# Performance work log

Hardware: AMD Instinct MI355X
Metric: run time of the kernel (lower is better)

Reference implementation:

```python
import jax, jax.numpy as jnp
import numpy as np

N = 4096        # num_node == num_hyperedge
IN_FT = 512
OUT_FT = 512
COS_THR = 0.5
COS_K = 10
SCALER = 1.0
EPS = 1e-12  # torch F.normalize eps


def _kaiming_uniform(key, shape, fan_in, a=2.0):
    # kaiming_uniform_ with a=sqrt(4)=2: gain = sqrt(2/(1+a^2)), bound = gain*sqrt(3/fan_in)
    gain = np.sqrt(2.0 / (1.0 + a * a))
    bound = gain * np.sqrt(3.0 / fan_in)
    return jax.random.uniform(key, shape, jnp.float32, -bound, bound)


def setup_inputs() -> dict:
    key = jax.random.key(0)
    k_x, k_w1, k_w2, k_pw, k_pb = jax.random.split(key, 5)
    x = jax.random.normal(k_x, (N, IN_FT), jnp.float32)
    H = jnp.ones((N, N), jnp.float32)  # initial full incidence, sparsified in forward
    weight1 = jnp.abs(_kaiming_uniform(k_w1, (N, N), fan_in=N))
    weight2 = jnp.abs(_kaiming_uniform(k_w2, (N, N), fan_in=N))
    proj_w = _kaiming_uniform(k_pw, (OUT_FT, IN_FT), fan_in=IN_FT)
    b = 1.0 / np.sqrt(IN_FT)
    proj_b = jax.random.uniform(k_pb, (OUT_FT,), jnp.float32, -b, b)
    return {"x": x, "H": H, "proj_w": proj_w, "proj_b": proj_b,
            "weight1": weight1, "weight2": weight2}


def reference(x, H, proj_w, proj_b, weight1, weight2):
    # --- dynamic hypergraph construction: cosine similarity + threshold/top-k mask ---
    xn = x / jnp.maximum(jnp.linalg.norm(x, axis=1, keepdims=True), 1e-12)
    cos = xn @ xn.T                                  # [N, N]
    mask = cos > COS_THR
    _, idx = jax.lax.top_k(cos, COS_K)               # [N, K] top-k per row
    rows = jnp.arange(N)[:, None]
    mask = mask.at[rows, idx].set(True)
    Hm = H * mask.astype(H.dtype)                    # sparsified incidence

    # --- projection ---
    h = x @ proj_w.T + proj_b                        # [N, out_ft]

    # --- node -> hyperedge aggregation ---
    nw = (weight1 * Hm).T                            # [E, N]
    nw = nw / jnp.maximum(jnp.sum(jnp.abs(nw), axis=1, keepdims=True), EPS) * SCALER
    h = nw @ h                                       # [E, out_ft]

    # --- hyperedge -> node aggregation ---
    hw = weight2 * Hm                                # [N, E]
    hw = hw / jnp.maximum(jnp.sum(jnp.abs(hw), axis=1, keepdims=True), EPS) * SCALER
    return hw @ h                                    # [N, out_ft]
```

## Files before the change

### kernel.cpp

```cpp
#include <hip/hip_runtime.h>
#include <hip/hip_bf16.h>
#include <math.h>

#define N 4096
#define IN_FT 512
#define OUT_FT 512
#define COS_THR 0.5f
#define COS_K 10
#define EPSN 1e-12f
#define CAP 256
#define NW (N / 32)
#define CAP_C 128
#define GAPWIN 1e-2f
#define CNB 32
#define T0 0.08f
#define SLOTS 24
#define NSLOT (32 * SLOTS)

typedef short s16x8 __attribute__((ext_vector_type(8)));
typedef float f32x4 __attribute__((ext_vector_type(4)));

__device__ __forceinline__ unsigned short f2bf(float f) {
    unsigned u = __float_as_uint(f);
    u += 0x7fff + ((u >> 16) & 1);
    return (unsigned short)(u >> 16);
}
__device__ __forceinline__ float bf2f(unsigned short h) {
    return __uint_as_float(((unsigned)h) << 16);
}
__device__ __forceinline__ void gload_lds16(const void* g, void* l) {
    __builtin_amdgcn_global_load_lds(
        (const __attribute__((address_space(1))) void*)g,
        (__attribute__((address_space(3))) void*)l, 16, 0, 0);
}

__global__ __launch_bounds__(256) void rownorm_k(const float* __restrict__ x,
                                                 unsigned short* __restrict__ xnh,
                                                 unsigned short* __restrict__ xnl,
                                                 float* __restrict__ norminv,
                                                 float* __restrict__ nrm,
                                                 int* __restrict__ fbflag) {
    int row = blockIdx.x;
    const float* xr = x + (size_t)row * IN_FT;
    float s = 0.f;
    for (int j = threadIdx.x; j < IN_FT; j += 256) { float v = xr[j]; s += v * v; }
    __shared__ float red[256];
    red[threadIdx.x] = s; __syncthreads();
    for (int off = 128; off > 0; off >>= 1) {
        if (threadIdx.x < off) red[threadIdx.x] += red[threadIdx.x + off];
        __syncthreads();
    }
    float nr = fmaxf(sqrtf(red[0]), 1e-12f);
    float inv = 1.0f / nr;
    if (threadIdx.x == 0) { norminv[row] = inv; nrm[row] = nr; fbflag[row] = 0; }
    for (int j = threadIdx.x; j < IN_FT; j += 256) {
        float v = xr[j] * inv;
        unsigned short hi = f2bf(v);
        unsigned short lo = f2bf(v - bf2f(hi));
        xnh[(size_t)row * IN_FT + j] = hi;
        xnl[(size_t)row * IN_FT + j] = lo;
    }
}

__global__ __launch_bounds__(256) void cos_gemm_k(const unsigned short* __restrict__ xh,
                                                  unsigned* __restrict__ cpack,
                                                  int* __restrict__ ccntg) {
    __shared__ __align__(16) unsigned short As[2][128 * 32];
    __shared__ __align__(16) unsigned short Bs[2][128 * 32];
    __shared__ int cntU[128], cntM[128];
    int bid = blockIdx.x;
    int t = (bid & 7) * 66 + (bid >> 3);
    int by = 0;
    while (t >= CNB - by) { t -= CNB - by; ++by; }
    int bx = by + t;
    int tid = threadIdx.x;
    int wave = tid >> 6, l = tid & 63;
    int bi = by * 128, bj = bx * 128;
    int wm = wave >> 1, wn = wave & 1;
    int lm0 = wm * 64, ln0 = wn * 64;
    int lr4 = l >> 2;
    int lc4s = (((l & 3) ^ ((l >> 3) & 3)) * 8);
    int lr = l & 15, lg = l >> 4;
    int kqs = (((l >> 4) ^ ((l >> 1) & 3)) * 8);
    f32x4 acc[4][4] = {};
    int buf = 0;
#pragma unroll
    for (int q = 0; q < 2; ++q) {
        int r0 = (wave + q * 4) * 16;
        gload_lds16(xh + (size_t)(bi + r0 + lr4) * IN_FT + lc4s, &As[0][r0 * 32]);
        gload_lds16(xh + (size_t)(bj + r0 + lr4) * IN_FT + lc4s, &Bs[0][r0 * 32]);
    }
    asm volatile("s_waitcnt vmcnt(0)" ::: "memory");
    __syncthreads();
    for (int kt = 0; kt < 16; ++kt) {
        if (kt + 1 < 16) {
            int kc = (kt + 1) * 32;
#pragma unroll
            for (int q = 0; q < 2; ++q) {
                int r0 = (wave + q * 4) * 16;
                gload_lds16(xh + (size_t)(bi + r0 + lr4) * IN_FT + kc + lc4s,
                            &As[buf ^ 1][r0 * 32]);
                gload_lds16(xh + (size_t)(bj + r0 + lr4) * IN_FT + kc + lc4s,
                            &Bs[buf ^ 1][r0 * 32]);
            }
        }
        s16x8 a[4], b[4];
#pragma unroll
        for (int mi = 0; mi < 4; ++mi)
            a[mi] = *(const s16x8*)&As[buf][(lm0 + mi * 16 + lr) * 32 + kqs];
#pragma unroll
        for (int ni = 0; ni < 4; ++ni)
            b[ni] = *(const s16x8*)&Bs[buf][(ln0 + ni * 16 + lr) * 32 + kqs];
#pragma unroll
        for (int mi = 0; mi < 4; ++mi)
#pragma unroll
            for (int ni = 0; ni < 4; ++ni)
                acc[mi][ni] = __builtin_amdgcn_mfma_f32_16x16x32_bf16(a[mi], b[ni], acc[mi][ni], 0, 0, 0);
        asm volatile("s_waitcnt vmcnt(0)" ::: "memory");
        __syncthreads();
        buf ^= 1;
    }
    if (tid < 128) { cntU[tid] = 0; cntM[tid] = 0; }
    __syncthreads();
#pragma unroll
    for (int mi = 0; mi < 4; ++mi)
#pragma unroll
        for (int r = 0; r < 4; ++r) {
            int rl = lm0 + mi * 16 + lg * 4 + r;
#pragma unroll
            for (int ni = 0; ni < 4; ++ni) {
                float val = acc[mi][ni][r];
                if (val > T0) {
                    int p = atomicAdd(&cntU[rl], 1);
                    if (p < SLOTS) {
                        int n = bj + ln0 + ni * 16 + lr;
                        size_t base = ((size_t)(bi + rl) * 32 + bx) * SLOTS + p;
                        cpack[base] = (__float_as_uint(val) & 0xFFFFF000u) | (unsigned)n;
                    }
                }
            }
        }
    if (bx != by) {
#pragma unroll
        for (int ni = 0; ni < 4; ++ni) {
            int rl2 = ln0 + ni * 16 + lr;
#pragma unroll
            for (int mi = 0; mi < 4; ++mi)
#pragma unroll
                for (int r = 0; r < 4; ++r) {
                    float val = acc[mi][ni][r];
                    if (val > T0) {
                        int p = atomicAdd(&cntM[rl2], 1);
                        if (p < SLOTS) {
                            int col = bi + lm0 + mi * 16 + lg * 4 + r;
                            size_t base = ((size_t)(bj + rl2) * 32 + by) * SLOTS + p;
                            cpack[base] = (__float_as_uint(val) & 0xFFFFF000u) | (unsigned)col;
                        }
                    }
                }
        }
    }
    __syncthreads();
    if (tid < 128) {
        ccntg[(size_t)(bi + tid) * 32 + bx] = cntU[tid];
        if (bx != by) ccntg[(size_t)(bj + tid) * 32 + by] = cntM[tid];
    }
}

__global__ __launch_bounds__(64) void topk_fast_k(const unsigned* __restrict__ cpack,
                                                  const int* __restrict__ ccntg,
                                                  const float* __restrict__ x,
                                                  const float* __restrict__ norminv,
                                                  unsigned* __restrict__ maskT,
                                                  const float* __restrict__ w2,
                                                  const float* __restrict__ Hmat,
                                                  int* __restrict__ rlist,
                                                  float* __restrict__ rval,
                                                  int* __restrict__ rcnt,
                                                  int* __restrict__ fbflag) {
    int row = blockIdx.x, lane = threadIdx.x;
    __shared__ int   cjj[CAP_C];
    __shared__ float exv[CAP_C];
    __shared__ unsigned char selw[CAP_C];
    __shared__ unsigned lmask[NW];
    __shared__ float xs[IN_FT];
    int cc = (lane < 32) ? ccntg[(size_t)row * 32 + lane] : 0;
    int sum = cc, mx = cc;
#pragma unroll
    for (int off = 32; off > 0; off >>= 1) {
        sum += __shfl_xor(sum, off);
        int m2 = __shfl_xor(mx, off);
        mx = m2 > mx ? m2 : mx;
    }
    if (mx > SLOTS || sum < COS_K) { if (lane == 0) fbflag[row] = 1; return; }
    const unsigned* cpr = cpack + (size_t)row * NSLOT;
    float cv[12]; int ci[12];
#pragma unroll
    for (int i = 0; i < 12; ++i) {
        unsigned u = cpr[lane + i * 64];
        float v = __uint_as_float(u & 0xFFFFF000u);
        bool ok = (v == v);
        cv[i] = ok ? v : -INFINITY;
        ci[i] = ok ? (int)(u & 0xFFFu) : 0x7fffffff;
    }
    int winr[10];
    float v10 = 0.f;
    unsigned exm = 0;
    for (int t = 0; t < COS_K; ++t) {
        float best = -INFINITY; int bidx = 0x7fffffff;
#pragma unroll
        for (int i = 0; i < 12; ++i)
            if (!((exm >> i) & 1) &&
                (cv[i] > best || (cv[i] == best && ci[i] < bidx))) { best = cv[i]; bidx = ci[i]; }
#pragma unroll
        for (int off = 32; off > 0; off >>= 1) {
            float v2 = __shfl_xor(best, off);
            int   i2 = __shfl_xor(bidx, off);
            if (v2 > best || (v2 == best && i2 < bidx)) { best = v2; bidx = i2; }
        }
#pragma unroll
        for (int i = 0; i < 12; ++i)
            if (ci[i] == bidx) exm |= 1u << i;
        winr[t] = bidx;
        if (t == COS_K - 1) v10 = best;
    }
    if (v10 - GAPWIN <= T0) { if (lane == 0) fbflag[row] = 1; return; }
    unsigned iswm = 0; int wc = 0;
    unsigned char flag[12];
#pragma unroll
    for (int i = 0; i < 12; ++i) {
        bool w = (cv[i] > v10 - GAPWIN) || (fabsf(cv[i] - COS_THR) < GAPWIN);
        if (w) { iswm |= 1u << i; ++wc; }
        bool iw = false;
#pragma unroll
        for (int t = 0; t < COS_K; ++t) iw |= (winr[t] == ci[i]);
        flag[i] = (cv[i] > COS_THR || iw) ? 1 : 0;
    }
    int scan = wc;
#pragma unroll
    for (int off = 1; off < 64; off <<= 1) {
        int nv = __shfl_up(scan, off);
        if (lane >= off) scan += nv;
    }
    int Mw = __shfl(scan, 63);
    if (Mw > CAP_C) { if (lane == 0) fbflag[row] = 1; return; }
    if (Mw > COS_K) {
        {
            const float4* xr4 = (const float4*)(x + (size_t)row * IN_FT);
            ((float4*)xs)[lane] = xr4[lane];
            ((float4*)xs)[lane + 64] = xr4[lane + 64];
        }
        int base = scan - wc;
        int mypos[12];
        {
            int pos = base;
#pragma unroll
            for (int i = 0; i < 12; ++i) {
                if ((iswm >> i) & 1) { cjj[pos] = ci[i]; mypos[i] = pos; ++pos; }
                else mypos[i] = -1;
            }
        }
        float invr = norminv[row];
        int grp = lane >> 4;
        int q = lane & 15;
        for (int mb = 0; mb < Mw; mb += 4) {
            int m = mb + grp;
            float part = 0.f;
            int j = (m < Mw) ? cjj[m] : cjj[0];
            float invj_ = norminv[j];
            const float4* xj4 = (const float4*)(x + (size_t)j * IN_FT);
            int kb = q * 32;
            float4 e0 = xj4[q * 8 + 0], e1 = xj4[q * 8 + 1];
            float4 e2 = xj4[q * 8 + 2], e3 = xj4[q * 8 + 3];
            float4 e4 = xj4[q * 8 + 4], e5 = xj4[q * 8 + 5];
            float4 e6 = xj4[q * 8 + 6], e7 = xj4[q * 8 + 7];
            const float4* f4s[8] = {&e0, &e1, &e2, &e3, &e4, &e5, &e6, &e7};
#pragma unroll
            for (int s = 0; s < 8; ++s) {
                float4 e = *f4s[s];
                part = fmaf(xs[kb + s * 4 + 0] * invr, e.x * invj_, part);
                part = fmaf(xs[kb + s * 4 + 1] * invr, e.y * invj_, part);
                part = fmaf(xs[kb + s * 4 + 2] * invr, e.z * invj_, part);
                part = fmaf(xs[kb + s * 4 + 3] * invr, e.w * invj_, part);
            }
#pragma unroll
            for (int off = 1; off < 16; off <<= 1)
                part += __shfl_xor(part, off);
            if (q == 0 && m < Mw) exv[m] = part;
        }
        for (int w = lane; w < Mw; w += 64) {
            float vv = exv[w]; int j = cjj[w];
            int rank = 0;
            for (int m2 = 0; m2 < Mw; ++m2) {
                float v2 = exv[m2]; int j2 = cjj[m2];
                if (v2 > vv || (v2 == vv && j2 < j)) ++rank;
            }
            selw[w] = (rank < COS_K) ? 1 : 0;
        }
#pragma unroll
        for (int i = 0; i < 12; ++i)
            if (mypos[i] >= 0)
                flag[i] = ((exv[mypos[i]] > COS_THR) || selw[mypos[i]]) ? 1 : 0;
    }
    lmask[lane] = 0; lmask[lane + 64] = 0;
#pragma unroll
    for (int i = 0; i < 12; ++i)
        if (flag[i]) atomicOr(&lmask[ci[i] >> 5], 1u << (ci[i] & 31));
    unsigned w0 = lmask[lane], w1 = lmask[lane + 64];
    maskT[(size_t)lane * N + row] = w0;
    maskT[(size_t)(lane + 64) * N + row] = w1;
    int c0 = __popc(w0), c1 = __popc(w1);
    int s0 = c0, s1 = c1;
#pragma unroll
    for (int off = 1; off < 64; off <<= 1) {
        int n0 = __shfl_up(s0, off);
        int n1 = __shfl_up(s1, off);
        if (lane >= off) { s0 += n0; s1 += n1; }
    }
    int tot0 = __shfl(s0, 63), tot1 = __shfl(s1, 63);
    int b0 = s0 - c0, b1 = tot0 + s1 - c1;
    {
        unsigned m = w0; int pos = b0;
        while (m) {
            int b = __builtin_ctz(m); m &= m - 1;
            int j = lane * 32 + b;
            if (pos < CAP) {
                size_t ofs = (size_t)row * N + j;
                rlist[(size_t)row * CAP + pos] = j;
                rval[(size_t)row * CAP + pos] = w2[ofs] * Hmat[ofs];
            }
            ++pos;
        }
        m = w1; pos = b1;
        while (m) {
            int b = __builtin_ctz(m); m &= m - 1;
            int j = (lane + 64) * 32 + b;
            if (pos < CAP) {
                size_t ofs = (size_t)row * N + j;
                rlist[(size_t)row * CAP + pos] = j;
                rval[(size_t)row * CAP + pos] = w2[ofs] * Hmat[ofs];
            }
            ++pos;
        }
    }
    if (lane == 0) {
        int tot = tot0 + tot1;
        rcnt[row] = tot < CAP ? tot : CAP;
    }
}

__global__ __launch_bounds__(256) void topk_fb_k(const int* __restrict__ fbflag,
                                                 const float* __restrict__ x,
                                                 const float* __restrict__ norminv,
                                                 unsigned* __restrict__ maskT,
                                                 const float* __restrict__ w2,
                                                 const float* __restrict__ Hmat,
                                                 int* __restrict__ rlist,
                                                 float* __restrict__ rval,
                                                 int* __restrict__ rcnt) {
    int row = blockIdx.x;
    if (!fbflag[row]) return;
    int tid = threadIdx.x;
    int lane = tid & 63, wid = tid >> 6;
    __shared__ float xrow[IN_FT];
    __shared__ float wv[4][10];
    __shared__ int   wi[4][10];
    __shared__ int   win[10];
    __shared__ int   wtot[4];
    const float* xr = x + (size_t)row * IN_FT;
    xrow[tid] = xr[tid]; xrow[tid + 256] = xr[tid + 256];
    __syncthreads();
    float invr = norminv[row];
    float v[16];
    const float4* xjp[16];
    float invj[16];
#pragma unroll
    for (int c = 0; c < 16; ++c) {
        int j = tid * 16 + c;
        xjp[c] = (const float4*)(x + (size_t)j * IN_FT);
        invj[c] = norminv[j];
        v[c] = 0.f;
    }
    for (int k4 = 0; k4 < IN_FT / 4; ++k4) {
        float xv0 = xrow[k4 * 4 + 0] * invr;
        float xv1 = xrow[k4 * 4 + 1] * invr;
        float xv2 = xrow[k4 * 4 + 2] * invr;
        float xv3 = xrow[k4 * 4 + 3] * invr;
#pragma unroll
        for (int c = 0; c < 16; ++c) {
            float4 e = xjp[c][k4];
            v[c] = fmaf(xv0, e.x * invj[c], v[c]);
            v[c] = fmaf(xv1, e.y * invj[c], v[c]);
            v[c] = fmaf(xv2, e.z * invj[c], v[c]);
            v[c] = fmaf(xv3, e.w * invj[c], v[c]);
        }
    }
    unsigned fl = 0;
#pragma unroll
    for (int c = 0; c < 16; ++c)
        if (v[c] > COS_THR) fl |= 1u << c;
    unsigned exm = 0;
#pragma unroll
    for (int t = 0; t < COS_K; ++t) {
        float best = -INFINITY; int bidx = 0x7fffffff;
#pragma unroll
        for (int c = 0; c < 16; ++c)
            if (!((exm >> c) & 1) && v[c] > best) { best = v[c]; bidx = tid * 16 + c; }
#pragma unroll
        for (int off = 32; off > 0; off >>= 1) {
            float v2 = __shfl_xor(best, off);
            int   i2 = __shfl_xor(bidx, off);
            if (v2 > best || (v2 == best && i2 < bidx)) { best = v2; bidx = i2; }
        }
        if ((bidx >> 4) == tid) exm |= 1u << (bidx & 15);
        if (lane == t) { wv[wid][t] = best; wi[wid][t] = bidx; }
    }
    __syncthreads();
    if (wid == 0) {
        float mv = -INFINITY; int mi = 0x7fffffff;
        if (lane < 40) { int g = lane / 10, s = lane - g * 10; mv = wv[g][s]; mi = wi[g][s]; }
        for (int t = 0; t < COS_K; ++t) {
            float best = mv; int bidx = mi;
#pragma unroll
            for (int off = 32; off > 0; off >>= 1) {
                float v2 = __shfl_xor(best, off);
                int   i2 = __shfl_xor(bidx, off);
                if (v2 > best || (v2 == best && i2 < bidx)) { best = v2; bidx = i2; }
            }
            if (mi == bidx) mv = -INFINITY;
            if (lane == 0) win[t] = bidx;
        }
    }
    __syncthreads();
#pragma unroll
    for (int t = 0; t < COS_K; ++t) {
        int wj = win[t];
        if ((wj >> 4) == tid) fl |= 1u << (wj & 15);
    }
    unsigned flp = __shfl_xor(fl, 1);
    if (!(tid & 1))
        maskT[(size_t)(tid >> 1) * N + row] = (fl & 0xffffu) | (flp << 16);
    int cnt = __popc(fl);
    int scan = cnt;
#pragma unroll
    for (int off = 1; off < 64; off <<= 1) {
        int nv = __shfl_up(scan, off);
        if (lane >= off) scan += nv;
    }
    if (lane == 63) wtot[wid] = scan;
    __syncthreads();
    int base = scan - cnt;
    for (int w = 0; w < wid; ++w) base += wtot[w];
    unsigned m = fl;
    int pos = base;
    while (m) {
        int c = __builtin_ctz(m); m &= m - 1;
        int j = tid * 16 + c;
        if (pos < CAP) {
            size_t ofs = (size_t)row * N + j;
            rlist[(size_t)row * CAP + pos] = j;
            rval[(size_t)row * CAP + pos] = w2[ofs] * Hmat[ofs];
        }
        ++pos;
    }
    if (tid == 0) {
        int tot = wtot[0] + wtot[1] + wtot[2] + wtot[3];
        rcnt[row] = tot < CAP ? tot : CAP;
    }
}

__global__ __launch_bounds__(256) void cast_w_k(const float* __restrict__ w,
                                                unsigned short* __restrict__ wh,
                                                unsigned short* __restrict__ wl) {
    int i4 = blockIdx.x * 256 + threadIdx.x;
    float4 f = ((const float4*)w)[i4];
    ushort4 hi, lo;
    hi.x = f2bf(f.x); lo.x = f2bf(f.x - bf2f(hi.x));
    hi.y = f2bf(f.y); lo.y = f2bf(f.y - bf2f(hi.y));
    hi.z = f2bf(f.z); lo.z = f2bf(f.z - bf2f(hi.z));
    hi.w = f2bf(f.w); lo.w = f2bf(f.w - bf2f(hi.w));
    ((ushort4*)wh)[i4] = hi;
    ((ushort4*)wl)[i4] = lo;
}

__global__ __launch_bounds__(256) void proj_mfma_k(const unsigned short* __restrict__ xh,
                                                   const unsigned short* __restrict__ xl,
                                                   const unsigned short* __restrict__ wh,
                                                   const unsigned short* __restrict__ wl,
                                                   const float* __restrict__ bias,
                                                   const float* __restrict__ nrm,
                                                   float* __restrict__ h) {
    int tid = threadIdx.x;
    int wave = tid >> 6, l = tid & 63;
    int m0 = blockIdx.y * 64 + wave * 16;
    int n0 = blockIdx.x * 64;
    int lr = l & 15;
    int kq = (l >> 4) * 8;
    const unsigned short* pah = xh + (size_t)(m0 + lr) * IN_FT + kq;
    const unsigned short* pal = xl + (size_t)(m0 + lr) * IN_FT + kq;
    f32x4 acc[4] = {};
    for (int k0 = 0; k0 < IN_FT; k0 += 32) {
        s16x8 ah = *(const s16x8*)(pah + k0);
        s16x8 al = *(const s16x8*)(pal + k0);
#pragma unroll
        for (int g = 0; g < 4; ++g) {
            const unsigned short* pbh = wh + (size_t)(n0 + g * 16 + lr) * IN_FT + kq + k0;
            const unsigned short* pbl = wl + (size_t)(n0 + g * 16 + lr) * IN_FT + kq + k0;
            s16x8 bh = *(const s16x8*)pbh;
            s16x8 bl = *(const s16x8*)pbl;
            acc[g] = __builtin_amdgcn_mfma_f32_16x16x32_bf16(ah, bh, acc[g], 0, 0, 0);
            acc[g] = __builtin_amdgcn_mfma_f32_16x16x32_bf16(ah, bl, acc[g], 0, 0, 0);
            acc[g] = __builtin_amdgcn_mfma_f32_16x16x32_bf16(al, bh, acc[g], 0, 0, 0);
        }
    }
#pragma unroll
    for (int g = 0; g < 4; ++g)
#pragma unroll
        for (int r = 0; r < 4; ++r) {
            int m = m0 + (l >> 4) * 4 + r;
            int n = n0 + g * 16 + lr;
            h[(size_t)m * OUT_FT + n] = nrm[m] * acc[g][r] + bias[n];
        }
}

__global__ __launch_bounds__(256) void count_cols_k(const unsigned* __restrict__ maskT,
                                                    int* __restrict__ cnt64) {
    __shared__ unsigned ch[512];
    int tid = threadIdx.x;
    int eb = blockIdx.x, chunk = blockIdx.y;
    int wbase = eb * 8, v0 = chunk * 64;
#pragma unroll
    for (int q = 0; q < 2; ++q) {
        int idx = tid + q * 256;
        int i = idx >> 6, r = idx & 63;
        ch[idx] = maskT[(size_t)(wbase + i) * N + v0 + r];
    }
    __syncthreads();
    int wl = tid >> 5, bp = tid & 31;
    int cnt = 0;
#pragma unroll
    for (int r = 0; r < 64; ++r) cnt += (ch[wl * 64 + r] >> bp) & 1;
    cnt64[chunk * N + eb * 256 + tid] = cnt;
}

__global__ __launch_bounds__(256) void fill_cols_k(const unsigned* __restrict__ maskT,
                                                   const int* __restrict__ cnt64,
                                                   const float* __restrict__ w1,
                                                   const float* __restrict__ Hmat,
                                                   int* __restrict__ elist,
                                                   float* __restrict__ eval_,
                                                   int* __restrict__ ecnt) {
    __shared__ unsigned ch[512];
    int tid = threadIdx.x;
    int eb = blockIdx.x, chunk = blockIdx.y;
    int e = eb * 256 + tid;
    int wbase = eb * 8, v0 = chunk * 64;
#pragma unroll
    for (int q = 0; q < 2; ++q) {
        int idx = tid + q * 256;
        int i = idx >> 6, r = idx & 63;
        ch[idx] = maskT[(size_t)(wbase + i) * N + v0 + r];
    }
    int pos = 0;
    for (int c = 0; c < chunk; ++c) pos += cnt64[c * N + e];
    __syncthreads();
    int wl = tid >> 5;
    unsigned bit = 1u << (tid & 31);
#pragma unroll
    for (int r = 0; r < 64; ++r) {
        if (ch[wl * 64 + r] & bit) {
            if (pos < CAP) {
                size_t ofs = (size_t)(v0 + r) * N + e;
                elist[(size_t)e * CAP + pos] = v0 + r;
                eval_[(size_t)e * CAP + pos] = w1[ofs] * Hmat[ofs];
            }
            ++pos;
        }
    }
    if (chunk == 63) ecnt[e] = pos < CAP ? pos : CAP;
}

__global__ __launch_bounds__(256) void spmm_k(const int* __restrict__ list,
                                              const float* __restrict__ val,
                                              const int* __restrict__ cnt,
                                              const float* __restrict__ src,
                                              float* __restrict__ dst) {
    int i = blockIdx.x;
    int f2 = threadIdx.x;
    int c = cnt[i];
    float ssum = 0.f;
    for (int t = 0; t < c; ++t) ssum += fabsf(val[(size_t)i * CAP + t]);
    float acc0 = 0.f, acc1 = 0.f;
    for (int t = 0; t < c; ++t) {
        int j = list[(size_t)i * CAP + t];
        float a = val[(size_t)i * CAP + t];
        float2 s = *(const float2*)&src[(size_t)j * OUT_FT + f2 * 2];
        acc0 += a * s.x;
        acc1 += a * s.y;
    }
    float sc = 1.0f / fmaxf(ssum, EPSN);
    float2 o = make_float2(acc0 * sc, acc1 * sc);
    *(float2*)&dst[(size_t)i * OUT_FT + f2 * 2] = o;
}

extern "C" void kernel_launch(void* const* d_in, const int* in_sizes, int n_in,
                              void* d_out, int out_size, void* d_ws, size_t ws_size,
                              hipStream_t stream) {
    const float* x      = (const float*)d_in[0];
    const float* Hmat   = (const float*)d_in[1];
    const float* proj_w = (const float*)d_in[2];
    const float* proj_b = (const float*)d_in[3];
    const float* w1     = (const float*)d_in[4];
    const float* w2     = (const float*)d_in[5];
    float* out = (float*)d_out;

    char* ws = (char*)d_ws;
    unsigned short* xnh     = (unsigned short*)(ws + 0);
    unsigned short* xnl     = (unsigned short*)(ws + 4194304);
    unsigned*       cpack   = (unsigned*)(ws + 8388608);
    int*            ccntg   = (int*)(ws + 20971520);
    float*          h       = (float*)(ws + 21495808);
    float*          h2      = (float*)(ws + 29884416);
    unsigned short* whi     = (unsigned short*)(ws + 38273024);
    unsigned short* wlo     = (unsigned short*)(ws + 38797312);
    unsigned*       maskT   = (unsigned*)(ws + 39321600);
    int*            cnt64   = (int*)(ws + 41418752);
    int*            ecnt    = (int*)(ws + 42467328);
    int*            rcnt    = (int*)(ws + 42483712);
    float*          norminv = (float*)(ws + 42500096);
    float*          nrm     = (float*)(ws + 42516480);
    int*            fbflag  = (int*)(ws + 42532864);
    int*            rlist   = (int*)(ws + 42549248);
    float*          rval    = (float*)(ws + 46743552);
    int*            elist   = (int*)(ws + 50937856);
    float*          eval_   = (float*)(ws + 55132160);

    hipMemsetAsync(cpack, 0xFF, (size_t)N * NSLOT * sizeof(unsigned), stream);
    rownorm_k<<<N, 256, 0, stream>>>(x, xnh, xnl, norminv, nrm, fbflag);
    cos_gemm_k<<<CNB * (CNB + 1) / 2, 256, 0, stream>>>(xnh, cpack, ccntg);
    topk_fast_k<<<N, 64, 0, stream>>>(cpack, ccntg, x, norminv, maskT,
                                      w2, Hmat, rlist, rval, rcnt, fbflag);
    topk_fb_k<<<N, 256, 0, stream>>>(fbflag, x, norminv, maskT,
                                     w2, Hmat, rlist, rval, rcnt);
    cast_w_k<<<256, 256, 0, stream>>>(proj_w, whi, wlo);
    proj_mfma_k<<<dim3(OUT_FT / 64, N / 64), 256, 0, stream>>>(xnh, xnl, whi, wlo,
                                                               proj_b, nrm, h);
    count_cols_k<<<dim3(16, 64), 256, 0, stream>>>(maskT, cnt64);
    fill_cols_k<<<dim3(16, 64), 256, 0, stream>>>(maskT, cnt64, w1, Hmat, elist, eval_, ecnt);
    spmm_k<<<N, 256, 0, stream>>>(elist, eval_, ecnt, h, h2);
    spmm_k<<<N, 256, 0, stream>>>(rlist, rval, rcnt, h2, out);
}
```

Baseline: 228.2 us.

## Split top-k selection into packed fast pass and separate fp32 refinement kernel

The per-row top-k kernel now packs four rows per 256-thread block. Rows whose candidates fall inside the ambiguity window no longer recompute exact fp32 dot products inline. Those rows write their window candidate list to global memory and are flagged for a new fix_k kernel. fix_k uses a full 256-thread block per flagged row to recompute the dot products, rank them, and rebuild that row's mask and lists. The intent is to remove the serial 64-thread tail from the common path and give the rare rows more parallelism. The cost is an extra kernel launch and extra global traffic for the flags and candidate lists.

```diff
diff --git a/kernel.cpp b/kernel.cpp
--- a/kernel.cpp
+++ b/kernel.cpp
@@ -39,7 +39,8 @@
                                                  unsigned short* __restrict__ xnl,
                                                  float* __restrict__ norminv,
                                                  float* __restrict__ nrm,
-                                                 int* __restrict__ fbflag) {
+                                                 int* __restrict__ fbflag,
+                                                 int* __restrict__ fixflg) {
     int row = blockIdx.x;
     const float* xr = x + (size_t)row * IN_FT;
     float s = 0.f;
@@ -52,7 +53,7 @@
     }
     float nr = fmaxf(sqrtf(red[0]), 1e-12f);
     float inv = 1.0f / nr;
-    if (threadIdx.x == 0) { norminv[row] = inv; nrm[row] = nr; fbflag[row] = 0; }
+    if (threadIdx.x == 0) { norminv[row] = inv; nrm[row] = nr; fbflag[row] = 0; fixflg[row] = 0; }
     for (int j = threadIdx.x; j < IN_FT; j += 256) {
         float v = xr[j] * inv;
         unsigned short hi = f2bf(v);
@@ -167,23 +168,22 @@
     }
 }
 
-__global__ __launch_bounds__(64) void topk_fast_k(const unsigned* __restrict__ cpack,
+__global__ __launch_bounds__(256) void topk_sel_k(const unsigned* __restrict__ cpack,
                                                   const int* __restrict__ ccntg,
-                                                  const float* __restrict__ x,
-                                                  const float* __restrict__ norminv,
                                                   unsigned* __restrict__ maskT,
                                                   const float* __restrict__ w2,
                                                   const float* __restrict__ Hmat,
                                                   int* __restrict__ rlist,
                                                   float* __restrict__ rval,
                                                   int* __restrict__ rcnt,
-                                                  int* __restrict__ fbflag) {
-    int row = blockIdx.x, lane = threadIdx.x;
-    __shared__ int   cjj[CAP_C];
-    __shared__ float exv[CAP_C];
-    __shared__ unsigned char selw[CAP_C];
-    __shared__ unsigned lmask[NW];
-    __shared__ float xs[IN_FT];
+                                                  int* __restrict__ fbflag,
+                                                  int* __restrict__ fixflg,
+                                                  int* __restrict__ wlistg,
+                                                  int* __restrict__ wMw) {
+    int wid = threadIdx.x >> 6, lane = threadIdx.x & 63;
+    int row = blockIdx.x * 4 + wid;
+    __shared__ unsigned lmask_s[4][NW];
+    unsigned* lmask = lmask_s[wid];
     int cc = (lane < 32) ? ccntg[(size_t)row * 32 + lane] : 0;
     int sum = cc, mx = cc;
 #pragma unroll
@@ -245,62 +245,15 @@
     int Mw = __shfl(scan, 63);
     if (Mw > CAP_C) { if (lane == 0) fbflag[row] = 1; return; }
     if (Mw > COS_K) {
-        {
-            const float4* xr4 = (const float4*)(x + (size_t)row * IN_FT);
-            ((float4*)xs)[lane] = xr4[lane];
-            ((float4*)xs)[lane + 64] = xr4[lane + 64];
-        }
-        int base = scan - wc;
-        int mypos[12];
-        {
-            int pos = base;
-#pragma unroll
-            for (int i = 0; i < 12; ++i) {
-                if ((iswm >> i) & 1) { cjj[pos] = ci[i]; mypos[i] = pos; ++pos; }
-                else mypos[i] = -1;
-            }
-        }
-        float invr = norminv[row];
-        int grp = lane >> 4;
-        int q = lane & 15;
-        for (int mb = 0; mb < Mw; mb += 4) {
-            int m = mb + grp;
-            float part = 0.f;
-            int j = (m < Mw) ? cjj[m] : cjj[0];
-            float invj_ = norminv[j];
-            const float4* xj4 = (const float4*)(x + (size_t)j * IN_FT);
-            int kb = q * 32;
-            float4 e0 = xj4[q * 8 + 0], e1 = xj4[q * 8 + 1];
-            float4 e2 = xj4[q * 8 + 2], e3 = xj4[q * 8 + 3];
-            float4 e4 = xj4[q * 8 + 4], e5 = xj4[q * 8 + 5];
-            float4 e6 = xj4[q * 8 + 6], e7 = xj4[q * 8 + 7];
-            const float4* f4s[8] = {&e0, &e1, &e2, &e3, &e4, &e5, &e6, &e7};
-#pragma unroll
-            for (int s = 0; s < 8; ++s) {
-                float4 e = *f4s[s];
-                part = fmaf(xs[kb + s * 4 + 0] * invr, e.x * invj_, part);
-                part = fmaf(xs[kb + s * 4 + 1] * invr, e.y * invj_, part);
-                part = fmaf(xs[kb + s * 4 + 2] * invr, e.z * invj_, part);
-                part = fmaf(xs[kb + s * 4 + 3] * invr, e.w * invj_, part);
-            }
-#pragma unroll
-            for (int off = 1; off < 16; off <<= 1)
-                part += __shfl_xor(part, off);
-            if (q == 0 && m < Mw) exv[m] = part;
-        }
-        for (int w = lane; w < Mw; w += 64) {
-            float vv = exv[w]; int j = cjj[w];
-            int rank = 0;
-            for (int m2 = 0; m2 < Mw; ++m2) {
-                float v2 = exv[m2]; int j2 = cjj[m2];
-                if (v2 > vv || (v2 == vv && j2 < j)) ++rank;
-            }
-            selw[w] = (rank < COS_K) ? 1 : 0;
-        }
+        int pos = scan - wc;
 #pragma unroll
         for (int i = 0; i < 12; ++i)
-            if (mypos[i] >= 0)
-                flag[i] = ((exv[mypos[i]] > COS_THR) || selw[mypos[i]]) ? 1 : 0;
+            if ((iswm >> i) & 1) {
+                if (pos < CAP_C) wlistg[(size_t)row * CAP_C + pos] = ci[i];
+                ++pos;
+            }
+        if (lane == 0) { wMw[row] = Mw; fixflg[row] = 1; }
+        return;
     }
     lmask[lane] = 0; lmask[lane + 64] = 0;
 #pragma unroll
@@ -346,6 +299,128 @@
     if (lane == 0) {
         int tot = tot0 + tot1;
         rcnt[row] = tot < CAP ? tot : CAP;
+    }
+}
+
+__global__ __launch_bounds__(256) void fix_k(const int* __restrict__ fixflg,
+                                             const int* __restrict__ wlistg,
+                                             const int* __restrict__ wMw,
+                                             const unsigned* __restrict__ cpack,
+                                             const float* __restrict__ x,
+                                             const float* __restrict__ norminv,
+                                             unsigned* __restrict__ maskT,
+                                             const float* __restrict__ w2,
+                                             const float* __restrict__ Hmat,
+                                             int* __restrict__ rlist,
+                                             float* __restrict__ rval,
+                                             int* __restrict__ rcnt) {
+    int row = blockIdx.x;
+    if (!fixflg[row]) return;
+    int tid = threadIdx.x;
+    int lane = tid & 63, wid = tid >> 6;
+    __shared__ float xs[IN_FT];
+    __shared__ int   cjj[CAP_C];
+    __shared__ float exv[CAP_C];
+    __shared__ unsigned char selw[CAP_C];
+    __shared__ unsigned lmask[NW];
+    int Mw = wMw[row];
+    if (tid < 128) ((float4*)xs)[tid] = ((const float4*)(x + (size_t)row * IN_FT))[tid];
+    if (tid < Mw) cjj[tid] = wlistg[(size_t)row * CAP_C + tid];
+    if (tid < NW) lmask[tid] = 0;
+    __syncthreads();
+    float invr = norminv[row];
+    int grp = tid >> 4;
+    int q = tid & 15;
+    for (int mb = 0; mb < Mw; mb += 16) {
+        int m = mb + grp;
+        float part = 0.f;
+        int j = (m < Mw) ? cjj[m] : cjj[0];
+        float invj_ = norminv[j];
+        const float4* xj4 = (const float4*)(x + (size_t)j * IN_FT);
+        int kb = q * 32;
+        float4 e0 = xj4[q * 8 + 0], e1 = xj4[q * 8 + 1];
+        float4 e2 = xj4[q * 8 + 2], e3 = xj4[q * 8 + 3];
+        float4 e4 = xj4[q * 8 + 4], e5 = xj4[q * 8 + 5];
+        float4 e6 = xj4[q * 8 + 6], e7 = xj4[q * 8 + 7];
+        const float4* f4s[8] = {&e0, &e1, &e2, &e3, &e4, &e5, &e6, &e7};
+#pragma unroll
+        for (int s = 0; s < 8; ++s) {
+            float4 e = *f4s[s];
+            part = fmaf(xs[kb + s * 4 + 0] * invr, e.x * invj_, part);
+            part = fmaf(xs[kb + s * 4 + 1] * invr, e.y * invj_, part);
+            part = fmaf(xs[kb + s * 4 + 2] * invr, e.z * invj_, part);
+            part = fmaf(xs[kb + s * 4 + 3] * invr, e.w * invj_, part);
+        }
+#pragma unroll
+        for (int off = 1; off < 16; off <<= 1)
+            part += __shfl_xor(part, off);
+        if (q == 0 && m < Mw) exv[m] = part;
+    }
+    __syncthreads();
+    if (tid < Mw) {
+        float vv = exv[tid]; int j = cjj[tid];
+        int rank = 0;
+        for (int m2 = 0; m2 < Mw; ++m2) {
+            float v2 = exv[m2]; int j2 = cjj[m2];
+            if (v2 > vv || (v2 == vv && j2 < j)) ++rank;
+        }
+        selw[tid] = (rank < COS_K) ? 1 : 0;
+    }
+    __syncthreads();
+    const unsigned* cpr = cpack + (size_t)row * NSLOT;
+    for (int s = tid; s < NSLOT; s += 256) {
+        unsigned u = cpr[s];
+        float v = __uint_as_float(u & 0xFFFFF000u);
+        if (v == v) {
+            int j = (int)(u & 0xFFFu);
+            int w = -1;
+            for (int m2 = 0; m2 < Mw; ++m2)
+                if (cjj[m2] == j) { w = m2; break; }
+            bool f = (w >= 0) ? ((exv[w] > COS_THR) || selw[w]) : (v > COS_THR);
+            if (f) atomicOr(&lmask[j >> 5], 1u << (j & 31));
+        }
+    }
+    __syncthreads();
+    if (wid == 0) {
+        unsigned w0 = lmask[lane], w1 = lmask[lane + 64];
+        maskT[(size_t)lane * N + row] = w0;
+        maskT[(size_t)(lane + 64) * N + row] = w1;
+        int c0 = __popc(w0), c1 = __popc(w1);
+        int s0 = c0, s1 = c1;
+#pragma unroll
+        for (int off = 1; off < 64; off <<= 1) {
+            int n0 = __shfl_up(s0, off);
+            int n1 = __shfl_up(s1, off);
+            if (lane >= off) { s0 += n0; s1 += n1; }
+        }
+        int tot0 = __shfl(s0, 63), tot1 = __shfl(s1, 63);
+        int b0 = s0 - c0, b1 = tot0 + s1 - c1;
+        unsigned m = w0; int pos = b0;
+        while (m) {
+            int b = __builtin_ctz(m); m &= m - 1;
+            int j = lane * 32 + b;
+            if (pos < CAP) {
+                size_t ofs = (size_t)row * N + j;
+                rlist[(size_t)row * CAP + pos] = j;
+                rval[(size_t)row * CAP + pos] = w2[ofs] * Hmat[ofs];
+            }
+            ++pos;
+        }
+        m = w1; pos = b1;
+        while (m) {
+            int b = __builtin_ctz(m); m &= m - 1;
+            int j = (lane + 64) * 32 + b;
+            if (pos < CAP) {
+                size_t ofs = (size_t)row * N + j;
+                rlist[(size_t)row * CAP + pos] = j;
+                rval[(size_t)row * CAP + pos] = w2[ofs] * Hmat[ofs];
+            }
+            ++pos;
+        }
+        if (lane == 0) {
+            int tot = tot0 + tot1;
+            rcnt[row] = tot < CAP ? tot : CAP;
+        }
     }
 }
 
@@ -630,16 +705,22 @@
     float*          norminv = (float*)(ws + 42500096);
     float*          nrm     = (float*)(ws + 42516480);
     int*            fbflag  = (int*)(ws + 42532864);
-    int*            rlist   = (int*)(ws + 42549248);
-    float*          rval    = (float*)(ws + 46743552);
-    int*            elist   = (int*)(ws + 50937856);
-    float*          eval_   = (float*)(ws + 55132160);
+    int*            fixflg  = (int*)(ws + 42549248);
+    int*            wMw     = (int*)(ws + 42565632);
+    int*            rlist   = (int*)(ws + 42582016);
+    float*          rval    = (float*)(ws + 46776320);
+    int*            elist   = (int*)(ws + 50970624);
+    float*          eval_   = (float*)(ws + 55164928);
+    int*            wlistg  = (int*)(ws + 59359232);
 
     hipMemsetAsync(cpack, 0xFF, (size_t)N * NSLOT * sizeof(unsigned), stream);
-    rownorm_k<<<N, 256, 0, stream>>>(x, xnh, xnl, norminv, nrm, fbflag);
+    rownorm_k<<<N, 256, 0, stream>>>(x, xnh, xnl, norminv, nrm, fbflag, fixflg);
     cos_gemm_k<<<CNB * (CNB + 1) / 2, 256, 0, stream>>>(xnh, cpack, ccntg);
-    topk_fast_k<<<N, 64, 0, stream>>>(cpack, ccntg, x, norminv, maskT,
-                                      w2, Hmat, rlist, rval, rcnt, fbflag);
+    topk_sel_k<<<N / 4, 256, 0, stream>>>(cpack, ccntg, maskT, w2, Hmat,
+                                          rlist, rval, rcnt, fbflag, fixflg,
+                                          wlistg, wMw);
+    fix_k<<<N, 256, 0, stream>>>(fixflg, wlistg, wMw, cpack, x, norminv,
+                                 maskT, w2, Hmat, rlist, rval, rcnt);
     topk_fb_k<<<N, 256, 0, stream>>>(fbflag, x, norminv, maskT,
                                      w2, Hmat, rlist, rval, rcnt);
     cast_w_k<<<256, 256, 0, stream>>>(proj_w, whi, wlo);
```

After: 263.8 us. 1.16x slower.
